# Kernel optimization log

Hardware: AMD Instinct MI355X
Metric: run time of the kernel (lower is better)

Reference implementation:

```python
import jax, jax.numpy as jnp
import numpy as np

E = 512   # embed_dim
H = 16    # num_heads
D = E // H  # head_dim = 32
L = 2048  # target (query) length
S = 2048  # source (stored pattern) length
N = 4     # batch
LN_EPS = 1e-5


def setup_inputs() -> dict:
    key = jax.random.key(0)
    ks = jax.random.split(key, 8)
    inv_sqrt_e = 1.0 / np.sqrt(E).astype(np.float32)
    return {
        "query": jax.random.normal(ks[0], (L, N, E), jnp.float32),
        "key_in": jax.random.normal(ks[1], (S, N, E), jnp.float32),
        "value": jax.random.normal(ks[2], (S, N, E), jnp.float32),
        "scaling": jax.random.uniform(ks[3], (H,), jnp.float32),  # per-head beta
        "in_proj_weight": jax.random.normal(ks[4], (3 * E, E), jnp.float32) * inv_sqrt_e,
        "in_proj_bias": jnp.zeros((3 * E,), jnp.float32),
        "p_norm_weight": jnp.ones((D,), jnp.float32),
        "p_norm_bias": jnp.zeros((D,), jnp.float32),
        "out_proj_weight": jax.random.normal(ks[5], (E, E), jnp.float32) * inv_sqrt_e,
        "out_proj_bias": jnp.zeros((E,), jnp.float32),
    }


def reference(query, key_in, value, scaling, in_proj_weight, in_proj_bias,
              p_norm_weight, p_norm_bias, out_proj_weight, out_proj_bias):
    Lq, Nb, Ed = query.shape
    Sk = key_in.shape[0]
    # split packed in-projection (torch Linear convention: y = x @ W^T + b)
    wq, wk, wv = jnp.split(in_proj_weight, 3, axis=0)
    bq, bk, bv = jnp.split(in_proj_bias, 3, axis=0)
    q = jnp.einsum('lne,fe->lnf', query, wq) + bq
    k = jnp.einsum('sne,fe->snf', key_in, wk) + bk
    v = jnp.einsum('sne,fe->snf', value, wv) + bv
    # (len, N, H*D) -> (N, H, len, D)
    q = q.reshape(Lq, Nb, H, D).transpose(1, 2, 0, 3)
    k = k.reshape(Sk, Nb, H, D).transpose(1, 2, 0, 3)
    v = v.reshape(Sk, Nb, H, D).transpose(1, 2, 0, 3)

    def pattern_norm(x):
        # affine LayerNorm over the association (head) dimension D
        mu = jnp.mean(x, axis=-1, keepdims=True)
        var = jnp.mean(jnp.square(x - mu), axis=-1, keepdims=True)
        return (x - mu) * jax.lax.rsqrt(var + LN_EPS) * p_norm_weight + p_norm_bias

    k = pattern_norm(k)
    v = pattern_norm(v)

    beta = scaling.reshape(1, H, 1, 1)  # per-head inverse-temperature
    scores = jnp.einsum('nhld,nhsd->nhls', q * beta, k)  # [N,H,L,S]
    attn = jax.nn.softmax(scores, axis=-1)  # single Hopfield update (update_steps_max=0)
    out = jnp.einsum('nhls,nhsd->nhld', attn, v)  # [N,H,L,D]
    out = out.transpose(2, 0, 1, 3).reshape(Lq, Nb, H * D)
    out = jnp.einsum('lnf,of->lno', out, out_proj_weight) + out_proj_bias
    return out  # (L, N, E)
```

## Files before the change

kernel.cpp:

```cpp
#include <hip/hip_runtime.h>
#include <cstdint>

#define LN_EPS 1e-5f

typedef _Float16 f16;
typedef _Float16 half4_t __attribute__((ext_vector_type(4)));
typedef _Float16 half8_t __attribute__((ext_vector_type(8)));
typedef __fp16 fp16v2 __attribute__((ext_vector_type(2)));
typedef float f32x4 __attribute__((ext_vector_type(4)));

__device__ __forceinline__ void gl_lds16(const void* g, void* l) {
    __builtin_amdgcn_global_load_lds(
        (__attribute__((address_space(1))) void*)(uintptr_t)g,
        (__attribute__((address_space(3))) void*)(uint32_t)(uintptr_t)l,
        16, 0, 0);
}

__device__ __forceinline__ half4_t pack4(float a, float b, float c, float d) {
    fp16v2 lo = __builtin_amdgcn_cvt_pkrtz(a, b);
    fp16v2 hi = __builtin_amdgcn_cvt_pkrtz(c, d);
    half4_t r;
    r[0] = (f16)lo[0]; r[1] = (f16)lo[1]; r[2] = (f16)hi[0]; r[3] = (f16)hi[1];
    return r;
}

__global__ void k_cast(const float* __restrict__ W1f, const float* __restrict__ W2f,
                       const float* __restrict__ Xq, const float* __restrict__ Xk,
                       const float* __restrict__ Xv,
                       f16* __restrict__ W1h, f16* __restrict__ W2h,
                       f16* __restrict__ Xh) {
    int t0 = blockIdx.x * blockDim.x + threadIdx.x;
    #pragma unroll
    for (int rep = 0; rep < 4; ++rep) {
        int t = t0 + rep * 851968;
        const float4* src;
        half4_t* dst;
        int idx;
        if (t < 196608)      { src = (const float4*)W1f; dst = (half4_t*)W1h; idx = t; }
        else if (t < 262144) { src = (const float4*)W2f; dst = (half4_t*)W2h; idx = t - 196608; }
        else {
            int u = t - 262144;
            int s = u >> 20;
            idx = u & 1048575;
            src = (s == 0) ? (const float4*)Xq : ((s == 1) ? (const float4*)Xk : (const float4*)Xv);
            dst = (half4_t*)(Xh + (size_t)s * 4194304);
        }
        float4 v = src[idx];
        dst[idx] = pack4(v.x, v.y, v.z, v.w);
    }
}

__global__ __launch_bounds__(256) void k_inproj(
    const f16* __restrict__ Xh, const f16* __restrict__ W1,
    const float* __restrict__ bias, const float* __restrict__ scaling,
    f16* __restrict__ Qg, f16* __restrict__ Kg, f16* __restrict__ Vg)
{
    __shared__ __align__(16) char pool[49152];

    const int tid = threadIdx.x;
    const int m0 = blockIdx.x * 128;
    const int f0 = blockIdx.y * 128;
    const int sec = f0 >> 9;
    const f16* X = Xh + (size_t)sec * 4194304;
    f16* Ob = (sec == 0) ? Qg : ((sec == 1) ? Kg : Vg);

    const int wid = tid >> 6, ln = tid & 63, l15 = ln & 15, quad = ln >> 4;
    const int wm = wid >> 1, wn = wid & 1;
    const int srow = ln >> 2, sco = (ln & 3) * 8;

    f32x4 z4 = {0.f, 0.f, 0.f, 0.f};
    f32x4 acc[4][4];
    #pragma unroll
    for (int i = 0; i < 4; ++i)
        #pragma unroll
        for (int j = 0; j < 4; ++j) acc[i][j] = z4;

    auto issue = [&](int kt, int slot) {
        const int k0 = kt * 32;
        f16* As = (f16*)(pool + slot * 16384);
        f16* Bs = (f16*)(pool + slot * 16384 + 8192);
        #pragma unroll
        for (int i = 0; i < 2; ++i) {
            int row = wid * 32 + i * 16 + srow;
            gl_lds16(W1 + (size_t)(f0 + row) * 512 + k0 + sco,
                     Bs + (wid * 32 + i * 16) * 32);
            gl_lds16(X + (size_t)(m0 + row) * 512 + k0 + sco,
                     As + (wid * 32 + i * 16) * 32);
        }
    };
    issue(0, 0);
    issue(1, 1);

    int slot = 0;
    for (int kt = 0; kt < 16; ++kt) {
        if (kt < 15) asm volatile("s_waitcnt vmcnt(4)" ::: "memory");
        else         asm volatile("s_waitcnt vmcnt(0)" ::: "memory");
        __builtin_amdgcn_s_barrier();

        if (kt < 14) {
            int nb = slot + 2; if (nb >= 3) nb -= 3;
            issue(kt + 2, nb);
        }

        const f16* As = (const f16*)(pool + slot * 16384);
        const f16* Bs = (const f16*)(pool + slot * 16384 + 8192);
        half8_t a[4], b[4];
        #pragma unroll
        for (int i = 0; i < 4; ++i)
            a[i] = *(const half8_t*)(As + (wm * 64 + i * 16 + l15) * 32 + quad * 8);
        #pragma unroll
        for (int j = 0; j < 4; ++j)
            b[j] = *(const half8_t*)(Bs + (wn * 64 + j * 16 + l15) * 32 + quad * 8);
        __builtin_amdgcn_s_setprio(1);
        #pragma unroll
        for (int i = 0; i < 4; ++i)
            #pragma unroll
            for (int j = 0; j < 4; ++j)
                acc[i][j] = __builtin_amdgcn_mfma_f32_16x16x32_f16(b[j], a[i], acc[i][j], 0, 0, 0);
        __builtin_amdgcn_s_setprio(0);

        slot = slot + 1; if (slot == 3) slot = 0;
    }

    __syncthreads();
    f16* Ep = (f16*)pool;

    #pragma unroll
    for (int j = 0; j < 4; ++j) {
        int floc0 = wn * 64 + j * 16 + quad * 4;
        int fb = f0 + floc0;
        int hh = (fb & 511) >> 5;
        float sc2 = (sec == 0) ? scaling[hh] * 1.44269504f : 1.0f;
        float4 bs4 = *(const float4*)(bias + fb);
        #pragma unroll
        for (int i = 0; i < 4; ++i) {
            int mloc = wm * 64 + i * 16 + l15;
            int key = (mloc >> 2) & 7;
            *(half4_t*)(Ep + mloc * 128 + (floc0 ^ (key << 3))) =
                pack4((acc[i][j][0] + bs4.x) * sc2, (acc[i][j][1] + bs4.y) * sc2,
                      (acc[i][j][2] + bs4.z) * sc2, (acc[i][j][3] + bs4.w) * sc2);
        }
    }
    __syncthreads();

    {
        int fgrp = (tid >> 6) * 4 + quad;
        int fs = (f0 & 511) + fgrp * 8;
        int hh = fs >> 5, cc = (fs >> 3) & 3;
        #pragma unroll
        for (int it = 0; it < 8; ++it) {
            int nb = it & 3, lblk = it >> 2;
            int L = lblk * 16 + l15;
            int mloc = nb + 4 * L;
            half8_t v = *(const half8_t*)(Ep + mloc * 128 + ((fgrp ^ (L & 7)) << 3));
            int gg = nb * 16 + hh;
            size_t l = (size_t)(m0 >> 2) + L;
            *(half8_t*)(Ob + (size_t)gg * 65536 + (size_t)cc * 16384 + l * 8) = v;
        }
    }
}

__global__ void k_norm_kv(f16* __restrict__ Kg, const f16* __restrict__ Vg,
                          const float* __restrict__ w, const float* __restrict__ b,
                          f16* __restrict__ Vtg) {
    __shared__ __align__(16) f16 T[32 * 64];
    const int t = threadIdx.x;
    const int seg = blockIdx.x, g = blockIdx.y;
    const int s_l = t >> 2, c = t & 3;
    const size_t base = (size_t)g * 65536 + (size_t)c * 16384 + (size_t)(seg * 64 + s_l) * 8;

    half8_t kv = *(const half8_t*)(Kg + base);
    half8_t vv = *(const half8_t*)(Vg + base);
    float kf[8], vf[8];
    float ks1 = 0.f, ks2 = 0.f, vs1 = 0.f, vs2 = 0.f;
    #pragma unroll
    for (int j = 0; j < 8; ++j) {
        kf[j] = (float)kv[j]; ks1 += kf[j]; ks2 += kf[j] * kf[j];
        vf[j] = (float)vv[j]; vs1 += vf[j]; vs2 += vf[j] * vf[j];
    }
    ks1 += __shfl_xor(ks1, 1); ks1 += __shfl_xor(ks1, 2);
    ks2 += __shfl_xor(ks2, 1); ks2 += __shfl_xor(ks2, 2);
    vs1 += __shfl_xor(vs1, 1); vs1 += __shfl_xor(vs1, 2);
    vs2 += __shfl_xor(vs2, 1); vs2 += __shfl_xor(vs2, 2);
    float kmu = ks1 * (1.f / 32.f), kvar = ks2 * (1.f / 32.f) - kmu * kmu;
    float vmu = vs1 * (1.f / 32.f), vvar = vs2 * (1.f / 32.f) - vmu * vmu;
    float krs = rsqrtf(kvar + LN_EPS), vrs = rsqrtf(vvar + LN_EPS);

    half8_t ky;
    int cs = s_l >> 3, es = s_l & 7;
    #pragma unroll
    for (int j = 0; j < 8; ++j) {
        int d = c * 8 + j;
        float wd = w[d], bd = b[d];
        ky[j] = (f16)((kf[j] - kmu) * krs * wd + bd);
        T[d * 64 + (cs ^ j) * 8 + es] = (f16)((vf[j] - vmu) * vrs * wd + bd);
    }
    *(half8_t*)(Kg + base) = ky;
    __syncthreads();
    int d_o = t >> 3, c_o = t & 7;
    half8_t out = *(const half8_t*)(T + d_o * 64 + c_o * 8);
    *(half8_t*)(Vtg + (size_t)(g * 32 + seg) * 2048 + d_o * 64 + c_o * 8) = out;
}

__global__ __launch_bounds__(256, 4) void k_flash(
    const f16* __restrict__ Qg, const f16* __restrict__ Kg,
    const f16* __restrict__ Vtg, f16* __restrict__ Og)
{
    __shared__ __align__(16) char smem[40960];

    const int tid = threadIdx.x, wid = tid >> 6, ln = tid & 63;
    const int l15 = ln & 15, quad = ln >> 4, l8 = ln & 7;
    char* Pw = smem + 24576 + wid * 4096;
    const int g = blockIdx.x, h = g & 15, n = g >> 4;
    const int q0 = blockIdx.y * 128;

    half8_t aq[2];
    #pragma unroll
    for (int i = 0; i < 2; ++i)
        aq[i] = *(const half8_t*)(Qg + (size_t)g * 65536 + (size_t)quad * 16384 +
                                  (size_t)(q0 + wid * 32 + i * 16 + l15) * 8);

    const f16* kp = Kg + (size_t)g * 65536 + (size_t)wid * 16384;
    const f16* vp = Vtg + (size_t)(g * 32) * 2048 + wid * 512;
    gl_lds16(kp + (size_t)ln * 8, smem + wid * 1024);
    gl_lds16(vp + (size_t)ln * 8, smem + 12288 + wid * 1024);
    gl_lds16(kp + 512 + (size_t)ln * 8, smem + 4096 + wid * 1024);
    gl_lds16(vp + 2048 + (size_t)ln * 8, smem + 12288 + 4096 + wid * 1024);
    kp += 1024;
    vp += 4096;

    half8_t onesf;
    {
        f16 o = (l15 == 0) ? (f16)1.0f : (f16)0.0f;
        #pragma unroll
        for (int j = 0; j < 8; ++j) onesf[j] = o;
    }

    f32x4 z4 = {0.f, 0.f, 0.f, 0.f};
    f32x4 accO[2][2], accSum[2];
    accO[0][0] = z4; accO[0][1] = z4; accO[1][0] = z4; accO[1][1] = z4;
    accSum[0] = z4; accSum[1] = z4;
    float m_i[2] = {-1e30f, -1e30f};

    int cur = 0;
    for (int st = 0; st < 32; ++st) {
        if (st < 31) asm volatile("s_waitcnt vmcnt(2)" ::: "memory");
        else         asm volatile("s_waitcnt vmcnt(0)" ::: "memory");
        __builtin_amdgcn_s_barrier();

        if (st < 30) {
            int nb = cur + 2; if (nb >= 3) nb -= 3;
            gl_lds16(kp + (size_t)ln * 8, smem + nb * 4096 + wid * 1024);
            gl_lds16(vp + (size_t)ln * 8, smem + 12288 + nb * 4096 + wid * 1024);
            kp += 512;
            vp += 2048;
        }
        const char* Kl = smem + cur * 4096;
        const char* Vt = smem + 12288 + cur * 4096;

        half8_t ak[4];
        #pragma unroll
        for (int mt = 0; mt < 4; ++mt)
            ak[mt] = *(const half8_t*)(Kl + quad * 1024 + (mt * 16 + l15) * 16);
        f32x4 accS[2][4];
        __builtin_amdgcn_s_setprio(1);
        #pragma unroll
        for (int i = 0; i < 2; ++i)
            #pragma unroll
            for (int mt = 0; mt < 4; ++mt)
                accS[i][mt] = __builtin_amdgcn_mfma_f32_16x16x32_f16(ak[mt], aq[i], z4, 0, 0, 0);
        __builtin_amdgcn_s_setprio(0);

        float mn[2];
        bool up = false;
        #pragma unroll
        for (int i = 0; i < 2; ++i) {
            float xm = fmaxf(fmaxf(accS[i][0][0], accS[i][0][1]),
                             fmaxf(accS[i][0][2], accS[i][0][3]));
            #pragma unroll
            for (int mt = 1; mt < 4; ++mt)
                xm = fmaxf(xm, fmaxf(fmaxf(accS[i][mt][0], accS[i][mt][1]),
                                     fmaxf(accS[i][mt][2], accS[i][mt][3])));
            xm = fmaxf(xm, __shfl_xor(xm, 16));
            xm = fmaxf(xm, __shfl_xor(xm, 32));
            up = up || (xm > m_i[i] + 8.f);
            mn[i] = fmaxf(m_i[i], xm);
        }
        if (__ballot(up)) {
            #pragma unroll
            for (int i = 0; i < 2; ++i) {
                float alpha = __builtin_amdgcn_exp2f(m_i[i] - mn[i]);
                #pragma unroll
                for (int dt = 0; dt < 2; ++dt)
                    #pragma unroll
                    for (int r = 0; r < 4; ++r) accO[i][dt][r] *= alpha;
                #pragma unroll
                for (int r = 0; r < 4; ++r) accSum[i][r] *= alpha;
                m_i[i] = mn[i];
            }
        }

        #pragma unroll
        for (int i = 0; i < 2; ++i) {
            #pragma unroll
            for (int mt = 0; mt < 4; ++mt) {
                float p0 = __builtin_amdgcn_exp2f(accS[i][mt][0] - m_i[i]);
                float p1 = __builtin_amdgcn_exp2f(accS[i][mt][1] - m_i[i]);
                float p2 = __builtin_amdgcn_exp2f(accS[i][mt][2] - m_i[i]);
                float p3 = __builtin_amdgcn_exp2f(accS[i][mt][3] - m_i[i]);
                int ch = (mt * 2 + (quad >> 1)) ^ l8;
                *(half4_t*)(Pw + (i * 16 + l15) * 128 + ch * 16 + (quad & 1) * 8) =
                    pack4(p0, p1, p2, p3);
            }
        }

        #pragma unroll
        for (int kt = 0; kt < 2; ++kt) {
            half8_t av[2], bp[2];
            #pragma unroll
            for (int dt = 0; dt < 2; ++dt) {
                int d = dt * 16 + l15;
                int cp = (kt * 4 + quad) ^ (l15 & 7);
                av[dt] = *(const half8_t*)(Vt + d * 128 + cp * 16);
            }
            #pragma unroll
            for (int i = 0; i < 2; ++i)
                bp[i] = *(const half8_t*)(Pw + (i * 16 + l15) * 128 +
                                          (((kt * 4 + quad) ^ l8) * 16));
            __builtin_amdgcn_s_setprio(1);
            #pragma unroll
            for (int i = 0; i < 2; ++i) {
                #pragma unroll
                for (int dt = 0; dt < 2; ++dt)
                    accO[i][dt] = __builtin_amdgcn_mfma_f32_16x16x32_f16(av[dt], bp[i], accO[i][dt], 0, 0, 0);
                accSum[i] = __builtin_amdgcn_mfma_f32_16x16x32_f16(onesf, bp[i], accSum[i], 0, 0, 0);
            }
            __builtin_amdgcn_s_setprio(0);
        }

        cur = cur + 1; if (cur == 3) cur = 0;
    }

    #pragma unroll
    for (int i = 0; i < 2; ++i) {
        float li = __shfl(accSum[i][0], l15);
        float inv = 1.f / li;
        #pragma unroll
        for (int dt = 0; dt < 2; ++dt)
            *(half4_t*)(Pw + (i * 16 + l15) * 80 + (dt * 16 + quad * 4) * 2) =
                pack4(accO[i][dt][0] * inv, accO[i][dt][1] * inv,
                      accO[i][dt][2] * inv, accO[i][dt][3] * inv);
    }
    int q2 = ln >> 1, hf = ln & 1;
    half8_t o0 = *(const half8_t*)(Pw + q2 * 80 + hf * 32);
    half8_t o1 = *(const half8_t*)(Pw + q2 * 80 + hf * 32 + 16);
    size_t rowe = ((size_t)(n * 2048 + q0 + wid * 32 + q2)) * 512 + h * 32 + hf * 16;
    *(half8_t*)(Og + rowe) = o0;
    *(half8_t*)(Og + rowe + 8) = o1;
}

__global__ __launch_bounds__(256) void k_outproj(
    const f16* __restrict__ A, const f16* __restrict__ W2,
    const float* __restrict__ bias, float* __restrict__ Out)
{
    __shared__ __align__(16) char pool[36864];

    const int tid = threadIdx.x;
    const int m0 = blockIdx.x * 64;
    const int f0 = blockIdx.y * 128;
    const int wid = tid >> 6, ln = tid & 63, l15 = ln & 15, quad = ln >> 4;
    const int wm = wid >> 1, wn = wid & 1;
    const int srow = ln >> 2, sco = (ln & 3) * 8;

    f32x4 z4 = {0.f, 0.f, 0.f, 0.f};
    f32x4 acc[2][4];
    #pragma unroll
    for (int i = 0; i < 2; ++i)
        #pragma unroll
        for (int j = 0; j < 4; ++j) acc[i][j] = z4;

    auto issue = [&](int kt, int slot) {
        const int k0 = kt * 32;
        f16* As = (f16*)(pool + slot * 12288);
        f16* Bs = (f16*)(pool + slot * 12288 + 4096);
        int arow = wid * 16 + srow;
        gl_lds16(A + (size_t)(m0 + arow) * 512 + k0 + sco,
                 As + wid * 512);
        #pragma unroll
        for (int i = 0; i < 2; ++i) {
            int brow = wid * 32 + i * 16 + srow;
            gl_lds16(W2 + (size_t)(f0 + brow) * 512 + k0 + sco,
                     Bs + (wid * 32 + i * 16) * 32);
        }
    };
    issue(0, 0);
    issue(1, 1);

    int slot = 0;
    for (int kt = 0; kt < 16; ++kt) {
        if (kt < 15) asm volatile("s_waitcnt vmcnt(3)" ::: "memory");
        else         asm volatile("s_waitcnt vmcnt(0)" ::: "memory");
        __builtin_amdgcn_s_barrier();

        if (kt < 14) {
            int nb = slot + 2; if (nb >= 3) nb -= 3;
            issue(kt + 2, nb);
        }

        const f16* As = (const f16*)(pool + slot * 12288);
        const f16* Bs = (const f16*)(pool + slot * 12288 + 4096);
        half8_t a[2], b[4];
        #pragma unroll
        for (int i = 0; i < 2; ++i)
            a[i] = *(const half8_t*)(As + (wm * 32 + i * 16 + l15) * 32 + quad * 8);
        #pragma unroll
        for (int j = 0; j < 4; ++j)
            b[j] = *(const half8_t*)(Bs + (wn * 64 + j * 16 + l15) * 32 + quad * 8);
        __builtin_amdgcn_s_setprio(1);
        #pragma unroll
        for (int i = 0; i < 2; ++i)
            #pragma unroll
            for (int j = 0; j < 4; ++j)
                acc[i][j] = __builtin_amdgcn_mfma_f32_16x16x32_f16(b[j], a[i], acc[i][j], 0, 0, 0);
        __builtin_amdgcn_s_setprio(0);

        slot = slot + 1; if (slot == 3) slot = 0;
    }

    __syncthreads();
    float* Ef = (float*)pool;

    #pragma unroll
    for (int j = 0; j < 4; ++j) {
        int floc0 = wn * 64 + j * 16 + quad * 4;
        float4 bs4 = *(const float4*)(bias + f0 + floc0);
        #pragma unroll
        for (int i = 0; i < 2; ++i) {
            int mloc = wm * 32 + i * 16 + l15;
            float4 o;
            o.x = acc[i][j][0] + bs4.x;
            o.y = acc[i][j][1] + bs4.y;
            o.z = acc[i][j][2] + bs4.z;
            o.w = acc[i][j][3] + bs4.w;
            *(float4*)(Ef + mloc * 132 + floc0) = o;
        }
    }
    __syncthreads();

    {
        int hw = tid >> 5, lane32 = tid & 31;
        #pragma unroll
        for (int it = 0; it < 8; ++it) {
            int row = it * 8 + hw;
            float4 v = *(const float4*)(Ef + row * 132 + lane32 * 4);
            int rm = m0 + row;
            int orow = (rm & 2047) * 4 + (rm >> 11);
            *(float4*)(Out + (size_t)orow * 512 + f0 + lane32 * 4) = v;
        }
    }
}

extern "C" void kernel_launch(void* const* d_in, const int* in_sizes, int n_in,
                              void* d_out, int out_size, void* d_ws, size_t ws_size,
                              hipStream_t stream) {
    const float* query   = (const float*)d_in[0];
    const float* key_in  = (const float*)d_in[1];
    const float* value   = (const float*)d_in[2];
    const float* scaling = (const float*)d_in[3];
    const float* ipw     = (const float*)d_in[4];
    const float* ipb     = (const float*)d_in[5];
    const float* pnw     = (const float*)d_in[6];
    const float* pnb     = (const float*)d_in[7];
    const float* opw     = (const float*)d_in[8];
    const float* opb     = (const float*)d_in[9];
    float* out = (float*)d_out;

    f16* Qg  = (f16*)d_ws;
    f16* Kg  = Qg + (size_t)4194304;
    f16* Vg  = Qg + (size_t)8388608;
    f16* W1  = Qg + (size_t)12582912;
    f16* W2  = Qg + (size_t)13369344;
    f16* Xh  = Qg + (size_t)13631488;
    f16* Vtg = Xh;
    f16* Og  = Vg;

    k_cast<<<3328, 256, 0, stream>>>(ipw, opw, query, key_in, value, W1, W2, Xh);
    k_inproj<<<dim3(64, 12), 256, 0, stream>>>(Xh, W1, ipb, scaling, Qg, Kg, Vg);
    k_norm_kv<<<dim3(32, 64), 256, 0, stream>>>(Kg, Vg, pnw, pnb, Vtg);
    k_flash<<<dim3(64, 16), 256, 0, stream>>>(Qg, Kg, Vtg, Og);
    k_outproj<<<dim3(128, 4), 256, 0, stream>>>(Og, W2, opb, out);
}
```

Baseline: 210.5 us.

## Fuse fp32-to-fp16 activation cast into in-projection GEMM A-tile loading

Result: slower. 221.3 us (+5.1%).

```diff
diff --git a/kernel.cpp b/kernel.cpp
--- a/kernel.cpp
+++ b/kernel.cpp
@@ -25,49 +25,39 @@
 }
 
 __global__ void k_cast(const float* __restrict__ W1f, const float* __restrict__ W2f,
-                       const float* __restrict__ Xq, const float* __restrict__ Xk,
-                       const float* __restrict__ Xv,
-                       f16* __restrict__ W1h, f16* __restrict__ W2h,
-                       f16* __restrict__ Xh) {
-    int t0 = blockIdx.x * blockDim.x + threadIdx.x;
-    #pragma unroll
-    for (int rep = 0; rep < 4; ++rep) {
-        int t = t0 + rep * 851968;
-        const float4* src;
-        half4_t* dst;
-        int idx;
-        if (t < 196608)      { src = (const float4*)W1f; dst = (half4_t*)W1h; idx = t; }
-        else if (t < 262144) { src = (const float4*)W2f; dst = (half4_t*)W2h; idx = t - 196608; }
-        else {
-            int u = t - 262144;
-            int s = u >> 20;
-            idx = u & 1048575;
-            src = (s == 0) ? (const float4*)Xq : ((s == 1) ? (const float4*)Xk : (const float4*)Xv);
-            dst = (half4_t*)(Xh + (size_t)s * 4194304);
-        }
-        float4 v = src[idx];
-        dst[idx] = pack4(v.x, v.y, v.z, v.w);
-    }
+                       f16* __restrict__ W1h, f16* __restrict__ W2h) {
+    int t = blockIdx.x * blockDim.x + threadIdx.x;
+    const float4* src;
+    half4_t* dst;
+    int idx;
+    if (t < 196608) { src = (const float4*)W1f; dst = (half4_t*)W1h; idx = t; }
+    else            { src = (const float4*)W2f; dst = (half4_t*)W2h; idx = t - 196608; }
+    float4 v = src[idx];
+    dst[idx] = pack4(v.x, v.y, v.z, v.w);
 }
 
 __global__ __launch_bounds__(256) void k_inproj(
-    const f16* __restrict__ Xh, const f16* __restrict__ W1,
+    const float* __restrict__ Xq, const float* __restrict__ Xk,
+    const float* __restrict__ Xv, const f16* __restrict__ W1,
     const float* __restrict__ bias, const float* __restrict__ scaling,
     f16* __restrict__ Qg, f16* __restrict__ Kg, f16* __restrict__ Vg)
 {
-    __shared__ __align__(16) char pool[49152];
+    __shared__ __align__(16) char pool[40960];
 
     const int tid = threadIdx.x;
     const int m0 = blockIdx.x * 128;
     const int f0 = blockIdx.y * 128;
     const int sec = f0 >> 9;
-    const f16* X = Xh + (size_t)sec * 4194304;
+    const float* X = (sec == 0) ? Xq : ((sec == 1) ? Xk : Xv);
     f16* Ob = (sec == 0) ? Qg : ((sec == 1) ? Kg : Vg);
 
     const int wid = tid >> 6, ln = tid & 63, l15 = ln & 15, quad = ln >> 4;
     const int wm = wid >> 1, wn = wid & 1;
     const int srow = ln >> 2, sco = (ln & 3) * 8;
 
+    const float* Xr0 = X + (size_t)(m0 + wid * 32 + srow) * 512 + sco;
+    const float* Xr1 = Xr0 + 16 * 512;
+
     f32x4 z4 = {0.f, 0.f, 0.f, 0.f};
     f32x4 acc[4][4];
     #pragma unroll
@@ -75,35 +65,59 @@
         #pragma unroll
         for (int j = 0; j < 4; ++j) acc[i][j] = z4;
 
-    auto issue = [&](int kt, int slot) {
+    auto issueB = [&](int kt, int slot) {
+        f16* Bs = (f16*)(pool + slot * 8192);
         const int k0 = kt * 32;
-        f16* As = (f16*)(pool + slot * 16384);
-        f16* Bs = (f16*)(pool + slot * 16384 + 8192);
         #pragma unroll
         for (int i = 0; i < 2; ++i) {
             int row = wid * 32 + i * 16 + srow;
             gl_lds16(W1 + (size_t)(f0 + row) * 512 + k0 + sco,
                      Bs + (wid * 32 + i * 16) * 32);
-            gl_lds16(X + (size_t)(m0 + row) * 512 + k0 + sco,
-                     As + (wid * 32 + i * 16) * 32);
         }
     };
-    issue(0, 0);
-    issue(1, 1);
-
-    int slot = 0;
-    for (int kt = 0; kt < 16; ++kt) {
-        if (kt < 15) asm volatile("s_waitcnt vmcnt(4)" ::: "memory");
+
+    issueB(0, 0);
+    float4 rA0 = *(const float4*)(Xr0);
+    float4 rA1 = *(const float4*)(Xr0 + 4);
+    float4 rA2 = *(const float4*)(Xr1);
+    float4 rA3 = *(const float4*)(Xr1 + 4);
+    issueB(1, 1);
+    float4 rB0 = *(const float4*)(Xr0 + 32);
+    float4 rB1 = *(const float4*)(Xr0 + 36);
+    float4 rB2 = *(const float4*)(Xr1 + 32);
+    float4 rB3 = *(const float4*)(Xr1 + 36);
+
+    auto bodyk = [&](int kt, int aslot, int bs,
+                     float4& r0, float4& r1, float4& r2, float4& r3) {
+        if (kt < 15) asm volatile("s_waitcnt vmcnt(6)" ::: "memory");
         else         asm volatile("s_waitcnt vmcnt(0)" ::: "memory");
+        {
+            f16* As = (f16*)(pool + 24576 + aslot * 8192);
+            half4_t lo = pack4(r0.x, r0.y, r0.z, r0.w);
+            half4_t hi = pack4(r1.x, r1.y, r1.z, r1.w);
+            half8_t h;
+            h[0] = lo[0]; h[1] = lo[1]; h[2] = lo[2]; h[3] = lo[3];
+            h[4] = hi[0]; h[5] = hi[1]; h[6] = hi[2]; h[7] = hi[3];
+            *(half8_t*)(As + (wid * 32 + srow) * 32 + sco) = h;
+            lo = pack4(r2.x, r2.y, r2.z, r2.w);
+            hi = pack4(r3.x, r3.y, r3.z, r3.w);
+            h[0] = lo[0]; h[1] = lo[1]; h[2] = lo[2]; h[3] = lo[3];
+            h[4] = hi[0]; h[5] = hi[1]; h[6] = hi[2]; h[7] = hi[3];
+            *(half8_t*)(As + (wid * 32 + 16 + srow) * 32 + sco) = h;
+        }
+        asm volatile("s_waitcnt lgkmcnt(0)" ::: "memory");
         __builtin_amdgcn_s_barrier();
-
         if (kt < 14) {
-            int nb = slot + 2; if (nb >= 3) nb -= 3;
-            issue(kt + 2, nb);
-        }
-
-        const f16* As = (const f16*)(pool + slot * 16384);
-        const f16* Bs = (const f16*)(pool + slot * 16384 + 8192);
+            int nb = bs + 2; if (nb >= 3) nb -= 3;
+            issueB(kt + 2, nb);
+            const int k2 = (kt + 2) * 32;
+            r0 = *(const float4*)(Xr0 + k2);
+            r1 = *(const float4*)(Xr0 + k2 + 4);
+            r2 = *(const float4*)(Xr1 + k2);
+            r3 = *(const float4*)(Xr1 + k2 + 4);
+        }
+        const f16* As = (const f16*)(pool + 24576 + aslot * 8192);
+        const f16* Bs = (const f16*)(pool + bs * 8192);
         half8_t a[4], b[4];
         #pragma unroll
         for (int i = 0; i < 4; ++i)
@@ -118,8 +132,15 @@
             for (int j = 0; j < 4; ++j)
                 acc[i][j] = __builtin_amdgcn_mfma_f32_16x16x32_f16(b[j], a[i], acc[i][j], 0, 0, 0);
         __builtin_amdgcn_s_setprio(0);
-
-        slot = slot + 1; if (slot == 3) slot = 0;
+    };
+
+    int bs = 0;
+    #pragma unroll 1
+    for (int it = 0; it < 8; ++it) {
+        bodyk(it * 2,     0, bs, rA0, rA1, rA2, rA3);
+        bs = (bs + 1 == 3) ? 0 : bs + 1;
+        bodyk(it * 2 + 1, 1, bs, rB0, rB1, rB2, rB3);
+        bs = (bs + 1 == 3) ? 0 : bs + 1;
     }
 
     __syncthreads();
@@ -480,12 +501,11 @@
     f16* Vg  = Qg + (size_t)8388608;
     f16* W1  = Qg + (size_t)12582912;
     f16* W2  = Qg + (size_t)13369344;
-    f16* Xh  = Qg + (size_t)13631488;
-    f16* Vtg = Xh;
+    f16* Vtg = Qg + (size_t)13631488;
     f16* Og  = Vg;
 
-    k_cast<<<3328, 256, 0, stream>>>(ipw, opw, query, key_in, value, W1, W2, Xh);
-    k_inproj<<<dim3(64, 12), 256, 0, stream>>>(Xh, W1, ipb, scaling, Qg, Kg, Vg);
+    k_cast<<<1024, 256, 0, stream>>>(ipw, opw, W1, W2);
+    k_inproj<<<dim3(64, 12), 256, 0, stream>>>(query, key_in, value, W1, ipb, scaling, Qg, Kg, Vg);
     k_norm_kv<<<dim3(32, 64), 256, 0, stream>>>(Kg, Vg, pnw, pnb, Vtg);
     k_flash<<<dim3(64, 16), 256, 0, stream>>>(Qg, Kg, Vtg, Og);
     k_outproj<<<dim3(128, 4), 256, 0, stream>>>(Og, W2, opb, out);
```

## Fuse K/V pattern LayerNorm and V transpose into in-projection epilogue

Applied to the files above, without the earlier changes.

After: 209.5 us. Within noise of the previous version (-0.5%).

```diff
diff --git a/kernel.cpp b/kernel.cpp
--- a/kernel.cpp
+++ b/kernel.cpp
@@ -53,16 +53,19 @@
 __global__ __launch_bounds__(256) void k_inproj(
     const f16* __restrict__ Xh, const f16* __restrict__ W1,
     const float* __restrict__ bias, const float* __restrict__ scaling,
-    f16* __restrict__ Qg, f16* __restrict__ Kg, f16* __restrict__ Vg)
+    const float* __restrict__ pnw, const float* __restrict__ pnb,
+    f16* __restrict__ Qg, f16* __restrict__ Kg, f16* __restrict__ Vtg)
 {
     __shared__ __align__(16) char pool[49152];
 
     const int tid = threadIdx.x;
-    const int m0 = blockIdx.x * 128;
-    const int f0 = blockIdx.y * 128;
+    const int bid = blockIdx.x;
+    const int jj = bid >> 3;
+    const int m0 = ((bid & 7) * 8 + (jj & 7)) * 128;
+    const int f0 = (jj >> 3) * 128;
     const int sec = f0 >> 9;
     const f16* X = Xh + (size_t)sec * 4194304;
-    f16* Ob = (sec == 0) ? Qg : ((sec == 1) ? Kg : Vg);
+    f16* Ob = (sec == 0) ? Qg : Kg;
 
     const int wid = tid >> 6, ln = tid & 63, l15 = ln & 15, quad = ln >> 4;
     const int wm = wid >> 1, wn = wid & 1;
@@ -125,25 +128,78 @@
     __syncthreads();
     f16* Ep = (f16*)pool;
 
-    #pragma unroll
-    for (int j = 0; j < 4; ++j) {
-        int floc0 = wn * 64 + j * 16 + quad * 4;
-        int fb = f0 + floc0;
-        int hh = (fb & 511) >> 5;
-        float sc2 = (sec == 0) ? scaling[hh] * 1.44269504f : 1.0f;
-        float4 bs4 = *(const float4*)(bias + fb);
-        #pragma unroll
-        for (int i = 0; i < 4; ++i) {
-            int mloc = wm * 64 + i * 16 + l15;
-            int key = (mloc >> 2) & 7;
+    float sA = 0.f, sB = 0.f;
+    float4 wA, wB, bA, bB;
+    if (sec == 0) {
+        int hbase = ((f0 & 511) >> 5) + wn * 2;
+        sA = scaling[hbase] * 1.44269504f;
+        sB = scaling[hbase + 1] * 1.44269504f;
+    } else {
+        wA = *(const float4*)(pnw + quad * 4);
+        wB = *(const float4*)(pnw + 16 + quad * 4);
+        bA = *(const float4*)(pnb + quad * 4);
+        bB = *(const float4*)(pnb + 16 + quad * 4);
+    }
+    float4 bias4[4];
+    #pragma unroll
+    for (int j = 0; j < 4; ++j)
+        bias4[j] = *(const float4*)(bias + f0 + wn * 64 + j * 16 + quad * 4);
+
+    #pragma unroll
+    for (int i = 0; i < 4; ++i) {
+        float x[4][4];
+        #pragma unroll
+        for (int j = 0; j < 4; ++j) {
+            x[j][0] = acc[i][j][0] + bias4[j].x;
+            x[j][1] = acc[i][j][1] + bias4[j].y;
+            x[j][2] = acc[i][j][2] + bias4[j].z;
+            x[j][3] = acc[i][j][3] + bias4[j].w;
+        }
+        if (sec == 0) {
+            #pragma unroll
+            for (int j = 0; j < 4; ++j) {
+                float sc = (j < 2) ? sA : sB;
+                #pragma unroll
+                for (int r = 0; r < 4; ++r) x[j][r] *= sc;
+            }
+        } else {
+            #pragma unroll
+            for (int hp = 0; hp < 2; ++hp) {
+                float s1 = 0.f, s2 = 0.f;
+                #pragma unroll
+                for (int jq = 0; jq < 2; ++jq) {
+                    int j = hp * 2 + jq;
+                    #pragma unroll
+                    for (int r = 0; r < 4; ++r) { s1 += x[j][r]; s2 += x[j][r] * x[j][r]; }
+                }
+                s1 += __shfl_xor(s1, 16); s1 += __shfl_xor(s1, 32);
+                s2 += __shfl_xor(s2, 16); s2 += __shfl_xor(s2, 32);
+                float mu = s1 * (1.f / 32.f);
+                float rs = rsqrtf(s2 * (1.f / 32.f) - mu * mu + LN_EPS);
+                #pragma unroll
+                for (int jq = 0; jq < 2; ++jq) {
+                    int j = hp * 2 + jq;
+                    const float4& wv = (j & 1) ? wB : wA;
+                    const float4& bv = (j & 1) ? bB : bA;
+                    x[j][0] = (x[j][0] - mu) * rs * wv.x + bv.x;
+                    x[j][1] = (x[j][1] - mu) * rs * wv.y + bv.y;
+                    x[j][2] = (x[j][2] - mu) * rs * wv.z + bv.z;
+                    x[j][3] = (x[j][3] - mu) * rs * wv.w + bv.w;
+                }
+            }
+        }
+        int mloc = wm * 64 + i * 16 + l15;
+        int key = (mloc >> 2) & 7;
+        #pragma unroll
+        for (int j = 0; j < 4; ++j) {
+            int floc0 = wn * 64 + j * 16 + quad * 4;
             *(half4_t*)(Ep + mloc * 128 + (floc0 ^ (key << 3))) =
-                pack4((acc[i][j][0] + bs4.x) * sc2, (acc[i][j][1] + bs4.y) * sc2,
-                      (acc[i][j][2] + bs4.z) * sc2, (acc[i][j][3] + bs4.w) * sc2);
+                pack4(x[j][0], x[j][1], x[j][2], x[j][3]);
         }
     }
     __syncthreads();
 
-    {
+    if (sec < 2) {
         int fgrp = (tid >> 6) * 4 + quad;
         int fs = (f0 & 511) + fgrp * 8;
         int hh = fs >> 5, cc = (fs >> 3) & 3;
@@ -157,49 +213,30 @@
             size_t l = (size_t)(m0 >> 2) + L;
             *(half8_t*)(Ob + (size_t)gg * 65536 + (size_t)cc * 16384 + l * 8) = v;
         }
-    }
-}
-
-__global__ void k_norm_kv(f16* __restrict__ Kg, const f16* __restrict__ Vg,
-                          const float* __restrict__ w, const float* __restrict__ b,
-                          f16* __restrict__ Vtg) {
-    __shared__ __align__(16) f16 T[32 * 64];
-    const int t = threadIdx.x;
-    const int seg = blockIdx.x, g = blockIdx.y;
-    const int s_l = t >> 2, c = t & 3;
-    const size_t base = (size_t)g * 65536 + (size_t)c * 16384 + (size_t)(seg * 64 + s_l) * 8;
-
-    half8_t kv = *(const half8_t*)(Kg + base);
-    half8_t vv = *(const half8_t*)(Vg + base);
-    float kf[8], vf[8];
-    float ks1 = 0.f, ks2 = 0.f, vs1 = 0.f, vs2 = 0.f;
-    #pragma unroll
-    for (int j = 0; j < 8; ++j) {
-        kf[j] = (float)kv[j]; ks1 += kf[j]; ks2 += kf[j] * kf[j];
-        vf[j] = (float)vv[j]; vs1 += vf[j]; vs2 += vf[j] * vf[j];
-    }
-    ks1 += __shfl_xor(ks1, 1); ks1 += __shfl_xor(ks1, 2);
-    ks2 += __shfl_xor(ks2, 1); ks2 += __shfl_xor(ks2, 2);
-    vs1 += __shfl_xor(vs1, 1); vs1 += __shfl_xor(vs1, 2);
-    vs2 += __shfl_xor(vs2, 1); vs2 += __shfl_xor(vs2, 2);
-    float kmu = ks1 * (1.f / 32.f), kvar = ks2 * (1.f / 32.f) - kmu * kmu;
-    float vmu = vs1 * (1.f / 32.f), vvar = vs2 * (1.f / 32.f) - vmu * vmu;
-    float krs = rsqrtf(kvar + LN_EPS), vrs = rsqrtf(vvar + LN_EPS);
-
-    half8_t ky;
-    int cs = s_l >> 3, es = s_l & 7;
-    #pragma unroll
-    for (int j = 0; j < 8; ++j) {
-        int d = c * 8 + j;
-        float wd = w[d], bd = b[d];
-        ky[j] = (f16)((kf[j] - kmu) * krs * wd + bd);
-        T[d * 64 + (cs ^ j) * 8 + es] = (f16)((vf[j] - vmu) * vrs * wd + bd);
-    }
-    *(half8_t*)(Kg + base) = ky;
-    __syncthreads();
-    int d_o = t >> 3, c_o = t & 7;
-    half8_t out = *(const half8_t*)(T + d_o * 64 + c_o * 8);
-    *(half8_t*)(Vtg + (size_t)(g * 32 + seg) * 2048 + d_o * 64 + c_o * 8) = out;
+    } else {
+        int seg = m0 >> 8;
+        int csb = ((m0 >> 7) & 1) * 4;
+        int hbase = (f0 & 511) >> 5;
+        #pragma unroll
+        for (int p = 0; p < 2; ++p) {
+            int idx = tid * 2 + p;
+            int g16 = idx >> 5, d = idx & 31;
+            int nb = g16 >> 2, hhl = g16 & 3;
+            int floc = hhl * 32 + d;
+            size_t obase = (size_t)((nb * 16 + hbase + hhl) * 32 + seg) * 2048 + d * 64;
+            #pragma unroll
+            for (int cq = 0; cq < 4; ++cq) {
+                half8_t hv;
+                #pragma unroll
+                for (int es = 0; es < 8; ++es) {
+                    int mloc = nb + 4 * (cq * 8 + es);
+                    hv[es] = Ep[mloc * 128 + (floc ^ (es << 3))];
+                }
+                int csx = (csb + cq) ^ (d & 7);
+                *(half8_t*)(Vtg + obase + csx * 8) = hv;
+            }
+        }
+    }
 }
 
 __global__ __launch_bounds__(256, 4) void k_flash(
@@ -477,16 +514,14 @@
 
     f16* Qg  = (f16*)d_ws;
     f16* Kg  = Qg + (size_t)4194304;
-    f16* Vg  = Qg + (size_t)8388608;
+    f16* Vtg = Qg + (size_t)8388608;
     f16* W1  = Qg + (size_t)12582912;
     f16* W2  = Qg + (size_t)13369344;
     f16* Xh  = Qg + (size_t)13631488;
-    f16* Vtg = Xh;
-    f16* Og  = Vg;
+    f16* Og  = Xh;
 
     k_cast<<<3328, 256, 0, stream>>>(ipw, opw, query, key_in, value, W1, W2, Xh);
-    k_inproj<<<dim3(64, 12), 256, 0, stream>>>(Xh, W1, ipb, scaling, Qg, Kg, Vg);
-    k_norm_kv<<<dim3(32, 64), 256, 0, stream>>>(Kg, Vg, pnw, pnb, Vtg);
+    k_inproj<<<768, 256, 0, stream>>>(Xh, W1, ipb, scaling, pnw, pnb, Qg, Kg, Vtg);
     k_flash<<<dim3(64, 16), 256, 0, stream>>>(Qg, Kg, Vtg, Og);
     k_outproj<<<dim3(128, 4), 256, 0, stream>>>(Og, W2, opb, out);
 }
```
